# Kernel tuning notes

Measured on AMD Instinct MI355X. Metric: run time of the kernel, lower is better.

## Reference

```python
import jax, jax.numpy as jnp
import numpy as np

B = 131072
HIDDEN = 256


def setup_inputs() -> dict:
    key = jax.random.key(0)
    ks = jax.random.split(key, 9)
    x = jax.random.uniform(ks[0], (B, 2), dtype=jnp.float32)
    # torch nn.Linear weights are [out_features, in_features]; kaiming-uniform-ish scale
    def w(k, out_f, in_f):
        bound = 1.0 / np.sqrt(in_f)
        return jax.random.uniform(k, (out_f, in_f), jnp.float32, -bound, bound)
    W0 = w(ks[1], HIDDEN, 2)
    W1 = w(ks[2], HIDDEN, HIDDEN)
    W2 = w(ks[3], HIDDEN, HIDDEN)
    W3 = w(ks[4], HIDDEN, HIDDEN)
    W4 = w(ks[5], HIDDEN, HIDDEN)
    W5 = w(ks[6], HIDDEN, HIDDEN)
    W6 = w(ks[7], HIDDEN, HIDDEN)
    W7 = w(ks[8], 3, HIDDEN)
    return {"x": x, "W0": W0, "W1": W1, "W2": W2, "W3": W3,
            "W4": W4, "W5": W5, "W6": W6, "W7": W7}


def reference(x, W0, W1, W2, W3, W4, W5, W6, W7):
    # 8 bias-free Linear layers: ReLU after layers 0..6, Sigmoid after layer 7.
    h = x
    for W in (W0, W1, W2, W3, W4, W5, W6):
        h = jax.nn.relu(h @ W.T)
    return jax.nn.sigmoid(h @ W7.T)  # [B, 3]
```

## Files before the change

### kernel.cpp

```cpp
#include <hip/hip_runtime.h>
#include <hip/hip_bf16.h>


#define HID 256
#define BM 64
#define NBLK 2048
#define HPITCH 264

typedef __attribute__((ext_vector_type(8))) short bf16x8;
typedef __attribute__((ext_vector_type(8))) unsigned short u16x8;
typedef __attribute__((ext_vector_type(4))) unsigned short u16x4;
typedef __attribute__((ext_vector_type(4))) float f32x4;

__device__ __forceinline__ unsigned short f2bf_rn(float f) {
    union { float f; unsigned u; } v; v.f = f;
    return (unsigned short)((v.u + 0x8000u) >> 16);
}
__device__ __forceinline__ float bf2f(unsigned short s) {
    union { unsigned u; float f; } v; v.u = ((unsigned)s) << 16;
    return v.f;
}
__device__ __forceinline__ unsigned cvt_pk_bf16(float lo, float hi) {
    unsigned r;
    asm("v_cvt_pk_bf16_f32 %0, %1, %2" : "=v"(r) : "v"(lo), "v"(hi));
    return r;
}

struct WPtrs { const float* w[6]; };

__global__ void pack_w_kernel(WPtrs wp, unsigned short* __restrict__ Wp) {
    int tid = blockIdx.x * 256 + threadIdx.x;
    int L   = tid >> 13;
    int rem = tid & 8191;
    int w   = rem >> 11;
    int kk  = (rem >> 8) & 7;
    int ft  = (rem >> 6) & 3;
    int l   = rem & 63;
    int n   = 64 * w + 16 * ft + (l & 15);
    int k0  = 32 * kk + 8 * (l >> 4);
    const float* src = wp.w[L] + n * HID + k0;
    u16x8 v;
#pragma unroll
    for (int j = 0; j < 8; ++j) {
        union { float f; unsigned u; } c; c.f = src[j];
        unsigned r = c.u + 0x7fffu + ((c.u >> 16) & 1u);
        v[j] = (unsigned short)(r >> 16);
    }
    *(u16x8*)(Wp + (size_t)tid * 8) = v;
}

__launch_bounds__(256, 3)
__global__ void mlp_fused_kernel(const float* __restrict__ x,
                                 const float* __restrict__ W0,
                                 const float* __restrict__ W7,
                                 const unsigned short* __restrict__ Wp,
                                 float* __restrict__ out) {
    __shared__ __align__(16) unsigned short Hs[BM][HPITCH];
    __shared__ float xs[BM][2];
    __shared__ float w7s[3 * HID];

    const int tid = threadIdx.x;
    const int l   = tid & 63;
    const int w   = tid >> 6;
    const int lr  = l & 15;
    const int lg  = l >> 4;
    const long r0 = (long)blockIdx.x * BM;

    const unsigned short* wbase = Wp + ((size_t)w << 14) + (size_t)l * 8;

    bf16x8 wb[2][4];
#pragma unroll
    for (int ft = 0; ft < 4; ++ft)
        wb[0][ft] = *(const bf16x8*)(wbase + ft * 512);

    if (tid < 2 * BM) ((float*)xs)[tid] = x[r0 * 2 + tid];
    w7s[tid]       = W7[tid];
    w7s[tid + 256] = W7[tid + 256];
    w7s[tid + 512] = W7[tid + 512];
    const float w00 = W0[2 * tid];
    const float w01 = W0[2 * tid + 1];
    __syncthreads();

#pragma unroll 8
    for (int m = 0; m < BM; ++m) {
        float h = fmaf(xs[m][0], w00, xs[m][1] * w01);
        Hs[m][tid] = f2bf_rn(fmaxf(0.f, h));
    }
    __syncthreads();

#pragma unroll
    for (int L = 0; L < 6; ++L) {
        f32x4 acc[4][4];
#pragma unroll
        for (int ft = 0; ft < 4; ++ft)
#pragma unroll
            for (int mt = 0; mt < 4; ++mt) acc[ft][mt] = (f32x4){0.f, 0.f, 0.f, 0.f};

#pragma unroll
        for (int kk = 0; kk < 8; ++kk) {
            const int cur = kk & 1, nxt = cur ^ 1;
            if (kk < 7) {
#pragma unroll
                for (int ft = 0; ft < 4; ++ft)
                    wb[nxt][ft] = *(const bf16x8*)(wbase + L * 65536 + (kk + 1) * 2048 + ft * 512);
            } else if (L < 5) {
#pragma unroll
                for (int ft = 0; ft < 4; ++ft)
                    wb[nxt][ft] = *(const bf16x8*)(wbase + (L + 1) * 65536 + ft * 512);
            }
            bf16x8 a[4];
#pragma unroll
            for (int mt = 0; mt < 4; ++mt)
                a[mt] = *(const bf16x8*)(&Hs[16 * mt + lr][32 * kk + 8 * lg]);
#pragma unroll
            for (int ft = 0; ft < 4; ++ft)
#pragma unroll
                for (int mt = 0; mt < 4; ++mt)
                    acc[ft][mt] = __builtin_amdgcn_mfma_f32_16x16x32_bf16(
                        wb[cur][ft], a[mt], acc[ft][mt], 0, 0, 0);
        }
        __syncthreads();
#pragma unroll
        for (int ft = 0; ft < 4; ++ft)
#pragma unroll
            for (int mt = 0; mt < 4; ++mt) {
                f32x4 v = acc[ft][mt];
                union { unsigned u[2]; u16x4 s; } pk;
                pk.u[0] = cvt_pk_bf16(fmaxf(0.f, v[0]), fmaxf(0.f, v[1]));
                pk.u[1] = cvt_pk_bf16(fmaxf(0.f, v[2]), fmaxf(0.f, v[3]));
                *(u16x4*)(&Hs[16 * mt + lr][64 * w + 16 * ft + 4 * lg]) = pk.s;
            }
        __syncthreads();
    }

    const int m = tid >> 2;
    const int q = tid & 3;
    float a0 = 0.f, a1 = 0.f, a2 = 0.f;
#pragma unroll
    for (int kb = 0; kb < 64; kb += 8) {
        u16x8 hv = *(const u16x8*)(&Hs[m][q * 64 + kb]);
#pragma unroll
        for (int j = 0; j < 8; ++j) {
            float h = bf2f(hv[j]);
            int k = q * 64 + kb + j;
            a0 = fmaf(h, w7s[k], a0);
            a1 = fmaf(h, w7s[HID + k], a1);
            a2 = fmaf(h, w7s[2 * HID + k], a2);
        }
    }
    a0 += __shfl_xor(a0, 1); a0 += __shfl_xor(a0, 2);
    a1 += __shfl_xor(a1, 1); a1 += __shfl_xor(a1, 2);
    a2 += __shfl_xor(a2, 1); a2 += __shfl_xor(a2, 2);
    if (q == 0) {
        long o = (r0 + m) * 3;
        out[o + 0] = 1.f / (1.f + __expf(-a0));
        out[o + 1] = 1.f / (1.f + __expf(-a1));
        out[o + 2] = 1.f / (1.f + __expf(-a2));
    }
}

extern "C" void kernel_launch(void* const* d_in, const int* in_sizes, int n_in,
                              void* d_out, int out_size, void* d_ws, size_t ws_size,
                              hipStream_t stream) {
    const float* x  = (const float*)d_in[0];
    const float* W0 = (const float*)d_in[1];
    WPtrs wp;
    for (int i = 0; i < 6; ++i) wp.w[i] = (const float*)d_in[2 + i];
    const float* W7 = (const float*)d_in[8];
    float* out = (float*)d_out;
    unsigned short* Wp = (unsigned short*)d_ws;

    pack_w_kernel<<<192, 256, 0, stream>>>(wp, Wp);
    mlp_fused_kernel<<<NBLK, 256, 0, stream>>>(x, W0, W7, Wp, out);
}
```

Measured before the change: 158.3 us.

## Switch hidden layers to 32x32x16 MFMA and compute final layer with MFMA

Hidden-layer GEMMs now use the 32x32x16 bf16 MFMA with a repacked weight layout, so fewer, larger matrix instructions run and fewer LDS activation loads and weight registers are needed per step. The final 3-output layer is packed to bf16 (zero-padded to 16 outputs) and computed with 16x16x32 MFMAs plus a small cross-wave reduction through shared memory, replacing scalar FMA loops. The first layer writes packed bf16 pairs, the layer loop is no longer unrolled, and occupancy is raised to 4 blocks per CU. The W7 product now takes bf16 weights, which adds rounding error, and the larger accumulators add register pressure against the higher occupancy target.

```diff
diff --git a/kernel.cpp b/kernel.cpp
--- a/kernel.cpp
+++ b/kernel.cpp
@@ -11,151 +11,161 @@
 typedef __attribute__((ext_vector_type(8))) unsigned short u16x8;
 typedef __attribute__((ext_vector_type(4))) unsigned short u16x4;
 typedef __attribute__((ext_vector_type(4))) float f32x4;
+typedef __attribute__((ext_vector_type(16))) float f32x16;
 
-__device__ __forceinline__ unsigned short f2bf_rn(float f) {
-    union { float f; unsigned u; } v; v.f = f;
-    return (unsigned short)((v.u + 0x8000u) >> 16);
-}
-__device__ __forceinline__ float bf2f(unsigned short s) {
-    union { unsigned u; float f; } v; v.u = ((unsigned)s) << 16;
-    return v.f;
-}
 __device__ __forceinline__ unsigned cvt_pk_bf16(float lo, float hi) {
     unsigned r;
     asm("v_cvt_pk_bf16_f32 %0, %1, %2" : "=v"(r) : "v"(lo), "v"(hi));
     return r;
 }
 
-struct WPtrs { const float* w[6]; };
+struct WPtrs { const float* w[6]; const float* w7; };
 
 __global__ void pack_w_kernel(WPtrs wp, unsigned short* __restrict__ Wp) {
     int tid = blockIdx.x * 256 + threadIdx.x;
-    int L   = tid >> 13;
-    int rem = tid & 8191;
-    int w   = rem >> 11;
-    int kk  = (rem >> 8) & 7;
-    int ft  = (rem >> 6) & 3;
-    int l   = rem & 63;
-    int n   = 64 * w + 16 * ft + (l & 15);
-    int k0  = 32 * kk + 8 * (l >> 4);
-    const float* src = wp.w[L] + n * HID + k0;
-    u16x8 v;
+    if (tid < 49152) {
+        int l  = tid & 63;
+        int ft = (tid >> 6) & 1;
+        int kk = (tid >> 7) & 15;
+        int w  = (tid >> 11) & 3;
+        int L  = tid >> 13;
+        int n  = 64 * w + 32 * ft + (l & 31);
+        int k0 = 16 * kk + 8 * (l >> 5);
+        const float* src = wp.w[L] + n * HID + k0;
+        u16x8 v;
 #pragma unroll
-    for (int j = 0; j < 8; ++j) {
-        union { float f; unsigned u; } c; c.f = src[j];
-        unsigned r = c.u + 0x7fffu + ((c.u >> 16) & 1u);
-        v[j] = (unsigned short)(r >> 16);
+        for (int j = 0; j < 8; ++j) {
+            union { float f; unsigned u; } c; c.f = src[j];
+            unsigned r = c.u + 0x7fffu + ((c.u >> 16) & 1u);
+            v[j] = (unsigned short)(r >> 16);
+        }
+        *(u16x8*)(Wp + (size_t)tid * 8) = v;
+    } else if (tid < 49664) {
+        int t  = tid - 49152;
+        int l  = t & 63;
+        int kk = t >> 6;
+        int n  = l & 15;
+        int k0 = 32 * kk + 8 * (l >> 4);
+        u16x8 v;
+#pragma unroll
+        for (int j = 0; j < 8; ++j) {
+            unsigned short s = 0;
+            if (n < 3) {
+                union { float f; unsigned u; } c; c.f = wp.w7[n * HID + k0 + j];
+                s = (unsigned short)((c.u + 0x7fffu + ((c.u >> 16) & 1u)) >> 16);
+            }
+            v[j] = s;
+        }
+        *(u16x8*)(Wp + 393216 + (size_t)t * 8) = v;
     }
-    *(u16x8*)(Wp + (size_t)tid * 8) = v;
 }
 
-__launch_bounds__(256, 3)
+__launch_bounds__(256, 4)
 __global__ void mlp_fused_kernel(const float* __restrict__ x,
                                  const float* __restrict__ W0,
-                                 const float* __restrict__ W7,
                                  const unsigned short* __restrict__ Wp,
                                  float* __restrict__ out) {
     __shared__ __align__(16) unsigned short Hs[BM][HPITCH];
-    __shared__ float xs[BM][2];
-    __shared__ float w7s[3 * HID];
+    __shared__ __align__(16) float Ps[4][64][4];
+    __shared__ float xsf[2 * BM];
 
     const int tid = threadIdx.x;
     const int l   = tid & 63;
     const int w   = tid >> 6;
-    const int lr  = l & 15;
-    const int lg  = l >> 4;
     const long r0 = (long)blockIdx.x * BM;
 
-    const unsigned short* wbase = Wp + ((size_t)w << 14) + (size_t)l * 8;
+    const unsigned short* wbl = Wp + (size_t)w * 16384 + (size_t)l * 8;
 
-    bf16x8 wb[2][4];
-#pragma unroll
-    for (int ft = 0; ft < 4; ++ft)
-        wb[0][ft] = *(const bf16x8*)(wbase + ft * 512);
+    bf16x8 wb[2][2];
+    wb[0][0] = *(const bf16x8*)(wbl);
+    wb[0][1] = *(const bf16x8*)(wbl + 512);
 
-    if (tid < 2 * BM) ((float*)xs)[tid] = x[r0 * 2 + tid];
-    w7s[tid]       = W7[tid];
-    w7s[tid + 256] = W7[tid + 256];
-    w7s[tid + 512] = W7[tid + 512];
-    const float w00 = W0[2 * tid];
-    const float w01 = W0[2 * tid + 1];
+    if (tid < 2 * BM) xsf[tid] = x[r0 * 2 + tid];
+    const int fp   = (tid & 127) * 2;
+    const int half = tid >> 7;
+    f32x4 w0v = *(const f32x4*)(W0 + 2 * fp);
     __syncthreads();
 
-#pragma unroll 8
-    for (int m = 0; m < BM; ++m) {
-        float h = fmaf(xs[m][0], w00, xs[m][1] * w01);
-        Hs[m][tid] = f2bf_rn(fmaxf(0.f, h));
+    const int mb = 32 * half;
+#pragma unroll
+    for (int i = 0; i < 32; ++i) {
+        int m = mb + i;
+        float x0 = xsf[2 * m], x1 = xsf[2 * m + 1];
+        float ha = fmaf(x0, w0v[0], x1 * w0v[1]);
+        float hb = fmaf(x0, w0v[2], x1 * w0v[3]);
+        *(unsigned*)(&Hs[m][fp]) = cvt_pk_bf16(fmaxf(0.f, ha), fmaxf(0.f, hb));
     }
     __syncthreads();
 
+    const int c  = l & 31;
+    const int hi = l >> 5;
+    for (int L = 0; L < 6; ++L) {
+        f32x16 acc[2][2];
 #pragma unroll
-    for (int L = 0; L < 6; ++L) {
-        f32x4 acc[4][4];
+        for (int ft = 0; ft < 2; ++ft)
 #pragma unroll
-        for (int ft = 0; ft < 4; ++ft)
+            for (int mt = 0; mt < 2; ++mt)
 #pragma unroll
-            for (int mt = 0; mt < 4; ++mt) acc[ft][mt] = (f32x4){0.f, 0.f, 0.f, 0.f};
+                for (int j = 0; j < 16; ++j) acc[ft][mt][j] = 0.f;
 
 #pragma unroll
-        for (int kk = 0; kk < 8; ++kk) {
+        for (int kk = 0; kk < 16; ++kk) {
             const int cur = kk & 1, nxt = cur ^ 1;
-            if (kk < 7) {
-#pragma unroll
-                for (int ft = 0; ft < 4; ++ft)
-                    wb[nxt][ft] = *(const bf16x8*)(wbase + L * 65536 + (kk + 1) * 2048 + ft * 512);
+            if (kk < 15) {
+                wb[nxt][0] = *(const bf16x8*)(wbl + L * 65536 + (kk + 1) * 1024);
+                wb[nxt][1] = *(const bf16x8*)(wbl + L * 65536 + (kk + 1) * 1024 + 512);
             } else if (L < 5) {
-#pragma unroll
-                for (int ft = 0; ft < 4; ++ft)
-                    wb[nxt][ft] = *(const bf16x8*)(wbase + (L + 1) * 65536 + ft * 512);
+                wb[nxt][0] = *(const bf16x8*)(wbl + (L + 1) * 65536);
+                wb[nxt][1] = *(const bf16x8*)(wbl + (L + 1) * 65536 + 512);
             }
-            bf16x8 a[4];
-#pragma unroll
-            for (int mt = 0; mt < 4; ++mt)
-                a[mt] = *(const bf16x8*)(&Hs[16 * mt + lr][32 * kk + 8 * lg]);
-#pragma unroll
-            for (int ft = 0; ft < 4; ++ft)
-#pragma unroll
-                for (int mt = 0; mt < 4; ++mt)
-                    acc[ft][mt] = __builtin_amdgcn_mfma_f32_16x16x32_bf16(
-                        wb[cur][ft], a[mt], acc[ft][mt], 0, 0, 0);
+            bf16x8 a0 = *(const bf16x8*)(&Hs[c][16 * kk + 8 * hi]);
+            bf16x8 a1 = *(const bf16x8*)(&Hs[32 + c][16 * kk + 8 * hi]);
+            acc[0][0] = __builtin_amdgcn_mfma_f32_32x32x16_bf16(wb[cur][0], a0, acc[0][0], 0, 0, 0);
+            acc[0][1] = __builtin_amdgcn_mfma_f32_32x32x16_bf16(wb[cur][0], a1, acc[0][1], 0, 0, 0);
+            acc[1][0] = __builtin_amdgcn_mfma_f32_32x32x16_bf16(wb[cur][1], a0, acc[1][0], 0, 0, 0);
+            acc[1][1] = __builtin_amdgcn_mfma_f32_32x32x16_bf16(wb[cur][1], a1, acc[1][1], 0, 0, 0);
         }
         __syncthreads();
 #pragma unroll
-        for (int ft = 0; ft < 4; ++ft)
+        for (int ft = 0; ft < 2; ++ft)
 #pragma unroll
-            for (int mt = 0; mt < 4; ++mt) {
-                f32x4 v = acc[ft][mt];
-                union { unsigned u[2]; u16x4 s; } pk;
-                pk.u[0] = cvt_pk_bf16(fmaxf(0.f, v[0]), fmaxf(0.f, v[1]));
-                pk.u[1] = cvt_pk_bf16(fmaxf(0.f, v[2]), fmaxf(0.f, v[3]));
-                *(u16x4*)(&Hs[16 * mt + lr][64 * w + 16 * ft + 4 * lg]) = pk.s;
+            for (int mt = 0; mt < 2; ++mt) {
+                f32x16 v = acc[ft][mt];
+#pragma unroll
+                for (int g = 0; g < 4; ++g) {
+                    union { unsigned u[2]; u16x4 s; } pk;
+                    pk.u[0] = cvt_pk_bf16(fmaxf(0.f, v[4 * g]),     fmaxf(0.f, v[4 * g + 1]));
+                    pk.u[1] = cvt_pk_bf16(fmaxf(0.f, v[4 * g + 2]), fmaxf(0.f, v[4 * g + 3]));
+                    *(u16x4*)(&Hs[32 * mt + c][64 * w + 32 * ft + 8 * g + 4 * hi]) = pk.s;
+                }
             }
         __syncthreads();
     }
 
-    const int m = tid >> 2;
-    const int q = tid & 3;
-    float a0 = 0.f, a1 = 0.f, a2 = 0.f;
+    const int lr = l & 15, lg = l >> 4;
+    const unsigned short* w7b = Wp + 393216 + (size_t)l * 8;
+    bf16x8 w7f0 = *(const bf16x8*)(w7b + (2 * w) * 512);
+    bf16x8 w7f1 = *(const bf16x8*)(w7b + (2 * w + 1) * 512);
+    f32x4 acc7[4];
 #pragma unroll
-    for (int kb = 0; kb < 64; kb += 8) {
-        u16x8 hv = *(const u16x8*)(&Hs[m][q * 64 + kb]);
+    for (int mt = 0; mt < 4; ++mt) acc7[mt] = (f32x4){0.f, 0.f, 0.f, 0.f};
 #pragma unroll
-        for (int j = 0; j < 8; ++j) {
-            float h = bf2f(hv[j]);
-            int k = q * 64 + kb + j;
-            a0 = fmaf(h, w7s[k], a0);
-            a1 = fmaf(h, w7s[HID + k], a1);
-            a2 = fmaf(h, w7s[2 * HID + k], a2);
-        }
+    for (int mt = 0; mt < 4; ++mt) {
+        bf16x8 a = *(const bf16x8*)(&Hs[16 * mt + lr][32 * (2 * w) + 8 * lg]);
+        acc7[mt] = __builtin_amdgcn_mfma_f32_16x16x32_bf16(w7f0, a, acc7[mt], 0, 0, 0);
+        bf16x8 b = *(const bf16x8*)(&Hs[16 * mt + lr][32 * (2 * w + 1) + 8 * lg]);
+        acc7[mt] = __builtin_amdgcn_mfma_f32_16x16x32_bf16(w7f1, b, acc7[mt], 0, 0, 0);
     }
-    a0 += __shfl_xor(a0, 1); a0 += __shfl_xor(a0, 2);
-    a1 += __shfl_xor(a1, 1); a1 += __shfl_xor(a1, 2);
-    a2 += __shfl_xor(a2, 1); a2 += __shfl_xor(a2, 2);
-    if (q == 0) {
-        long o = (r0 + m) * 3;
-        out[o + 0] = 1.f / (1.f + __expf(-a0));
-        out[o + 1] = 1.f / (1.f + __expf(-a1));
-        out[o + 2] = 1.f / (1.f + __expf(-a2));
+    if (lg == 0) {
+#pragma unroll
+        for (int mt = 0; mt < 4; ++mt)
+            *(f32x4*)(&Ps[w][16 * mt + lr][0]) = acc7[mt];
+    }
+    __syncthreads();
+    if (tid < 192) {
+        int row = tid / 3, o = tid - 3 * row;
+        float s = Ps[0][row][o] + Ps[1][row][o] + Ps[2][row][o] + Ps[3][row][o];
+        out[r0 * 3 + tid] = 1.f / (1.f + __expf(-s));
     }
 }
 
@@ -166,10 +176,10 @@
     const float* W0 = (const float*)d_in[1];
     WPtrs wp;
     for (int i = 0; i < 6; ++i) wp.w[i] = (const float*)d_in[2 + i];
-    const float* W7 = (const float*)d_in[8];
+    wp.w7 = (const float*)d_in[8];
     float* out = (float*)d_out;
     unsigned short* Wp = (unsigned short*)d_ws;
 
-    pack_w_kernel<<<192, 256, 0, stream>>>(wp, Wp);
-    mlp_fused_kernel<<<NBLK, 256, 0, stream>>>(x, W0, W7, Wp, out);
+    pack_w_kernel<<<194, 256, 0, stream>>>(wp, Wp);
+    mlp_fused_kernel<<<NBLK, 256, 0, stream>>>(x, W0, Wp, out);
 }
```

Result: slower. 163.5 us (+3.2%).
